# Optimization experiments

Measured on AMD Instinct MI355X. Metric: run time of the kernel, lower is better.

## Reference

```python
import jax, jax.numpy as jnp
import numpy as np
import math

D_MODEL = 1024
N_HEADS = 16
D_K = D_MODEL // N_HEADS
THETA = 0.1


def setup_inputs() -> dict:
    key = jax.random.key(0)
    ks = jax.random.split(key, 6)
    scale = np.sqrt(1.0 / D_MODEL).astype(np.float32)
    x = jax.random.normal(ks[0], (4, 2048, D_MODEL), dtype=jnp.float32)
    W_q = jax.random.normal(ks[1], (D_MODEL, D_MODEL), dtype=jnp.float32) * scale
    W_k = jax.random.normal(ks[2], (D_MODEL, D_MODEL), dtype=jnp.float32) * scale
    W_v = jax.random.normal(ks[3], (D_MODEL, D_MODEL), dtype=jnp.float32) * scale
    W_o = jax.random.normal(ks[4], (D_MODEL, D_MODEL), dtype=jnp.float32) * scale
    alpha = jnp.ones((1,), dtype=jnp.float32)
    return {"x": x, "W_q": W_q, "W_k": W_k, "W_v": W_v, "W_o": W_o, "alpha": alpha}


def reference(x, W_q, W_k, W_v, W_o, alpha):
    B, S, _ = x.shape
    Q = x @ W_q
    K = x @ W_k
    V = x @ W_v
    # non-commutative elementwise transforms
    Q = Q + THETA * jnp.sin(Q)
    K = K + THETA * jnp.cos(K)
    V = V + alpha * THETA * jnp.tanh(V)
    # split heads: [B, H, S, d_k]
    def split(t):
        return t.reshape(B, S, N_HEADS, D_K).transpose(0, 2, 1, 3)
    Qh, Kh, Vh = split(Q), split(K), split(V)
    scores = jnp.einsum('bhqd,bhkd->bhqk', Qh, Kh) / math.sqrt(D_K)
    attn = jax.nn.softmax(scores, axis=-1)
    out = jnp.einsum('bhqk,bhkd->bhqd', attn, Vh)
    out = out.transpose(0, 2, 1, 3).reshape(B, S, D_MODEL)
    return out @ W_o
```

## Files before the change

kernel.cpp:

```cpp
#include <hip/hip_runtime.h>

typedef __bf16 bf16x8 __attribute__((ext_vector_type(8)));
typedef float f32x4 __attribute__((ext_vector_type(4)));
typedef float f32x16 __attribute__((ext_vector_type(16)));

#define MFMA16(a,b,c) __builtin_amdgcn_mfma_f32_16x16x32_bf16(a,b,c,0,0,0)
#define MFMA32(a,b,c) __builtin_amdgcn_mfma_f32_32x32x16_bf16(a,b,c,0,0,0)

__device__ __forceinline__ unsigned short f2bf(float f) {
  unsigned int u = __float_as_uint(f);
  u = (u + 0x7FFFu + ((u >> 16) & 1u)) >> 16;
  return (unsigned short)u;
}

__device__ __forceinline__ void gload16(const void* g, void* l) {
  __builtin_amdgcn_global_load_lds(
      (const __attribute__((address_space(1))) void*)g,
      (__attribute__((address_space(3))) void*)l, 16, 0, 0);
}

__device__ __forceinline__ float vexp2(float x) {
  float r;
  asm("v_exp_f32 %0, %1" : "=v"(r) : "v"(x));
  return r;
}

__device__ __forceinline__ bf16x8 mk_pfrag(int hi, float p0, float p1, float p2, float p3,
                                           float p4, float p5, float p6, float p7) {
  unsigned int a0, a1, b0, b1;
  asm("v_cvt_pk_bf16_f32 %0, %1, %2" : "=v"(a0) : "v"(p0), "v"(p1));
  asm("v_cvt_pk_bf16_f32 %0, %1, %2" : "=v"(a1) : "v"(p2), "v"(p3));
  asm("v_cvt_pk_bf16_f32 %0, %1, %2" : "=v"(b0) : "v"(p4), "v"(p5));
  asm("v_cvt_pk_bf16_f32 %0, %1, %2" : "=v"(b1) : "v"(p6), "v"(p7));
  unsigned int x = __shfl_xor(hi ? a0 : b0, 32);
  unsigned int y = __shfl_xor(hi ? a1 : b1, 32);
  uint4 w;
  w.x = hi ? x : a0;
  w.y = hi ? y : a1;
  w.z = hi ? b0 : x;
  w.w = hi ? b1 : y;
  return *reinterpret_cast<bf16x8*>(&w);
}

__global__ __launch_bounds__(256) void k_convx(const float* __restrict__ x,
                                               unsigned short* __restrict__ xb) {
  int i = (blockIdx.x * 256 + threadIdx.x) * 4;
  float4 v = *reinterpret_cast<const float4*>(x + i);
  ushort4 o;
  o.x = f2bf(v.x); o.y = f2bf(v.y); o.z = f2bf(v.z); o.w = f2bf(v.w);
  *reinterpret_cast<ushort4*>(xb + i) = o;
}

__global__ __launch_bounds__(256) void k_transw(const float* __restrict__ W,
                                                unsigned short* __restrict__ WT) {
  __shared__ float t[32][33];
  int bx = blockIdx.x * 32;
  int by = blockIdx.y * 32;
  int tx = threadIdx.x & 31;
  int ty = threadIdx.x >> 5;
#pragma unroll
  for (int i = 0; i < 32; i += 8)
    t[ty + i][tx] = W[(size_t)(by + ty + i) * 1024 + bx + tx];
  __syncthreads();
#pragma unroll
  for (int i = 0; i < 32; i += 8)
    WT[(size_t)(bx + ty + i) * 1024 + by + tx] = f2bf(t[tx][ty + i]);
}

template <int EPI>
__global__ __launch_bounds__(256) void k_gemm(
    const unsigned short* __restrict__ A, const unsigned short* __restrict__ BT, int K,
    unsigned short* __restrict__ Qf, unsigned short* __restrict__ Kf,
    unsigned short* __restrict__ Vf, const float* __restrict__ alphaPtr,
    float* __restrict__ Out) {
  __shared__ __align__(16) unsigned short smem[128 * 136];
  unsigned short* AsBase = smem;
  unsigned short* BsBase = smem + 128 * 32;
  const int tid = threadIdx.x;
  const int wave = tid >> 6, lane = tid & 63;
  const int l15 = lane & 15, lg = lane >> 4;
  const int wr = wave >> 1, wc = wave & 1;
  const int bm = blockIdx.x, bn = blockIdx.y;

  f32x4 acc[4][4] = {};
  const unsigned short* Ab = A + (size_t)bm * 128 * K;
  const unsigned short* Bb = BT + (size_t)bn * 128 * K;

  const int r0 = tid >> 2, q0 = (tid & 3) * 8;
  const int r1 = r0 + 64;
  char* ldsA = (char*)AsBase + wave * 1024;
  char* ldsB = (char*)BsBase + wave * 1024;

  for (int k0 = 0; k0 < K; k0 += 32) {
    gload16((const void*)(Ab + (size_t)r0 * K + k0 + q0), ldsA);
    gload16((const void*)(Ab + (size_t)r1 * K + k0 + q0), ldsA + 4096);
    gload16((const void*)(Bb + (size_t)r0 * K + k0 + q0), ldsB);
    gload16((const void*)(Bb + (size_t)r1 * K + k0 + q0), ldsB + 4096);
    __syncthreads();
    bf16x8 af[4], bfr[4];
#pragma unroll
    for (int mi = 0; mi < 4; ++mi)
      af[mi] = *reinterpret_cast<const bf16x8*>(&AsBase[(wr * 64 + mi * 16 + l15) * 32 + lg * 8]);
#pragma unroll
    for (int ni = 0; ni < 4; ++ni)
      bfr[ni] = *reinterpret_cast<const bf16x8*>(&BsBase[(wc * 64 + ni * 16 + l15) * 32 + lg * 8]);
#pragma unroll
    for (int mi = 0; mi < 4; ++mi)
#pragma unroll
      for (int ni = 0; ni < 4; ++ni)
        acc[mi][ni] = MFMA16(af[mi], bfr[ni], acc[mi][ni]);
    __syncthreads();
  }

  if (EPI == 0) {
    const float av = alphaPtr[0];
    const int t = bn >> 3;
#pragma unroll
    for (int mi = 0; mi < 4; ++mi)
#pragma unroll
      for (int ni = 0; ni < 4; ++ni)
#pragma unroll
        for (int r = 0; r < 4; ++r) {
          int row = wr * 64 + mi * 16 + lg * 4 + r;
          int col = wc * 64 + ni * 16 + l15;
          float v = acc[mi][ni][r];
          if (t == 0) v += 0.1f * __sinf(v);
          else if (t == 1) v += 0.1f * __cosf(v);
          else {
            float e = __expf(2.0f * v);
            v += av * 0.1f * (1.0f - 2.0f * __builtin_amdgcn_rcpf(e + 1.0f));
          }
          smem[row * 136 + col] = f2bf(v);
        }
    __syncthreads();
    unsigned short* dst = (t == 0) ? Qf : (t == 1) ? Kf : Vf;
    const int c16 = tid & 15, rb = tid >> 4;
    const int ncol0 = (bn & 7) * 128;
#pragma unroll
    for (int i2 = 0; i2 < 8; ++i2) {
      int srow = rb + i2 * 16;
      uint4 val = *reinterpret_cast<const uint4*>(&smem[srow * 136 + c16 * 8]);
      *reinterpret_cast<uint4*>(dst + (size_t)(bm * 128 + srow) * 1024 + ncol0 + c16 * 8) = val;
    }
  } else {
#pragma unroll
    for (int ni = 0; ni < 4; ++ni) {
      int n = bn * 128 + wc * 64 + ni * 16 + l15;
#pragma unroll
      for (int mi = 0; mi < 4; ++mi) {
        int row = bm * 128 + wr * 64 + mi * 16 + lg * 4;
#pragma unroll
        for (int r = 0; r < 4; ++r)
          Out[(size_t)(row + r) * 1024 + n] = acc[mi][ni][r];
      }
    }
  }
}

__global__ __launch_bounds__(256)
__attribute__((amdgpu_waves_per_eu(4, 4)))
void k_attn(const unsigned short* __restrict__ Qf,
            const unsigned short* __restrict__ Kf,
            const unsigned short* __restrict__ Vf,
            unsigned short* __restrict__ AO) {
  __shared__ __align__(16) unsigned short smem[2 * (4096 + 4608)];
  const int tid = threadIdx.x;
  const int wave = tid >> 6, lane = tid & 63;
  const int l31 = lane & 31, hi = lane >> 5;
  const int f = (blockIdx.y << 4) | blockIdx.x;
  const int nf = ((f & 7) << 7) | (f >> 3);
  const int qb = nf & 15, bh = nf >> 4;
  const int b = bh >> 4, h = bh & 15;

  const unsigned short* Qb = Qf + ((size_t)b * 2048 + qb * 128 + wave * 32) * 1024 + h * 64;
  const unsigned short* Kb = Kf + (size_t)b * 2048 * 1024 + h * 64;
  const unsigned short* Vb = Vf + (size_t)b * 2048 * 1024 + h * 64;

  bf16x8 qfr[4];
#pragma unroll
  for (int ds = 0; ds < 4; ++ds)
    qfr[ds] = *reinterpret_cast<const bf16x8*>(Qb + (size_t)l31 * 1024 + ds * 16 + hi * 8);

  float lsum = 0.f;
  f32x16 o0 = {}, o1 = {};

  const int krow0 = wave * 16 + (lane >> 3);
  const int ksrcc = ((lane & 7) ^ (lane >> 3)) << 3;
  const int kxor = l31 & 7;

  const int sr = tid >> 3, sc = (tid & 7) * 8;
  const int u8 = tid & 7;
  const int swz0 = (l31 >> 3) << 3;
  const int swz1 = ((l31 >> 3) ^ 4) << 3;

  const float C1 = 0.18033688011112042f;

  uint4 va0, va1;
  va0 = *reinterpret_cast<const uint4*>(Vb + (size_t)sr * 1024 + sc);
  va1 = *reinterpret_cast<const uint4*>(Vb + (size_t)(sr + 32) * 1024 + sc);

  {
    unsigned short* Ks = smem;
    unsigned short* VT = smem + 4096;
    gload16((const void*)(Kb + (size_t)krow0 * 1024 + ksrcc), (char*)Ks + wave * 2048);
    gload16((const void*)(Kb + (size_t)(krow0 + 8) * 1024 + ksrcc), (char*)Ks + wave * 2048 + 1024);
    unsigned int w0[4] = {va0.x, va0.y, va0.z, va0.w};
    unsigned int w1[4] = {va1.x, va1.y, va1.z, va1.w};
#pragma unroll
    for (int e = 0; e < 4; ++e) {
      int d = sc + 2 * e;
      VT[(d * 72 + sr) ^ (u8 << 3)] = (unsigned short)w0[e];
      VT[((d + 1) * 72 + sr) ^ (u8 << 3)] = (unsigned short)(w0[e] >> 16);
      VT[(d * 72 + sr + 32) ^ (u8 << 3)] = (unsigned short)w1[e];
      VT[((d + 1) * 72 + sr + 32) ^ (u8 << 3)] = (unsigned short)(w1[e] >> 16);
    }
  }
  __syncthreads();

  for (int t = 0; t < 32; ++t) {
    unsigned short* KsC = smem + (t & 1) * 8704;
    unsigned short* VTC = KsC + 4096;
    unsigned short* KsN = smem + ((t + 1) & 1) * 8704;
    unsigned short* VTN = KsN + 4096;

    if (t < 31) {
      int kn = (t + 1) * 64;
      gload16((const void*)(Kb + (size_t)(kn + krow0) * 1024 + ksrcc), (char*)KsN + wave * 2048);
      gload16((const void*)(Kb + (size_t)(kn + krow0 + 8) * 1024 + ksrcc),
              (char*)KsN + wave * 2048 + 1024);
      va0 = *reinterpret_cast<const uint4*>(Vb + (size_t)(kn + sr) * 1024 + sc);
      va1 = *reinterpret_cast<const uint4*>(Vb + (size_t)(kn + sr + 32) * 1024 + sc);
    }

    f32x16 s0 = {}, s1 = {};
    __builtin_amdgcn_s_setprio(1);
#pragma unroll
    for (int ds = 0; ds < 4; ++ds) {
      int ch = ((ds * 2 + hi) ^ kxor) * 8;
      bf16x8 kf0 = *reinterpret_cast<const bf16x8*>(&KsC[l31 * 64 + ch]);
      bf16x8 kf1 = *reinterpret_cast<const bf16x8*>(&KsC[(l31 + 32) * 64 + ch]);
      s0 = MFMA32(kf0, qfr[ds], s0);
      s1 = MFMA32(kf1, qfr[ds], s1);
    }
    __builtin_amdgcn_s_setprio(0);

    float rs0 = 0.f, rs1 = 0.f, rs2 = 0.f, rs3 = 0.f;
#pragma unroll
    for (int r = 0; r < 16; r += 4) {
      float p0 = vexp2(s0[r] * C1);     s0[r] = p0;     rs0 += p0;
      float p1 = vexp2(s0[r + 1] * C1); s0[r + 1] = p1; rs1 += p1;
      float p2 = vexp2(s0[r + 2] * C1); s0[r + 2] = p2; rs2 += p2;
      float p3 = vexp2(s0[r + 3] * C1); s0[r + 3] = p3; rs3 += p3;
    }
#pragma unroll
    for (int r = 0; r < 16; r += 4) {
      float p0 = vexp2(s1[r] * C1);     s1[r] = p0;     rs0 += p0;
      float p1 = vexp2(s1[r + 1] * C1); s1[r + 1] = p1; rs1 += p1;
      float p2 = vexp2(s1[r + 2] * C1); s1[r + 2] = p2; rs2 += p2;
      float p3 = vexp2(s1[r + 3] * C1); s1[r + 3] = p3; rs3 += p3;
    }
    lsum += (rs0 + rs1) + (rs2 + rs3);

    if (t < 31) {
      unsigned int w0[4] = {va0.x, va0.y, va0.z, va0.w};
      unsigned int w1[4] = {va1.x, va1.y, va1.z, va1.w};
#pragma unroll
      for (int e = 0; e < 4; ++e) {
        int d = sc + 2 * e;
        VTN[(d * 72 + sr) ^ (u8 << 3)] = (unsigned short)w0[e];
        VTN[((d + 1) * 72 + sr) ^ (u8 << 3)] = (unsigned short)(w0[e] >> 16);
        VTN[(d * 72 + sr + 32) ^ (u8 << 3)] = (unsigned short)w1[e];
        VTN[((d + 1) * 72 + sr + 32) ^ (u8 << 3)] = (unsigned short)(w1[e] >> 16);
      }
    }

    __builtin_amdgcn_s_setprio(1);
#pragma unroll
    for (int ks = 0; ks < 4; ++ks) {
      bf16x8 pf =
          (ks == 0) ? mk_pfrag(hi, s0[0], s0[1], s0[2], s0[3], s0[4], s0[5], s0[6], s0[7])
        : (ks == 1) ? mk_pfrag(hi, s0[8], s0[9], s0[10], s0[11], s0[12], s0[13], s0[14], s0[15])
        : (ks == 2) ? mk_pfrag(hi, s1[0], s1[1], s1[2], s1[3], s1[4], s1[5], s1[6], s1[7])
                    : mk_pfrag(hi, s1[8], s1[9], s1[10], s1[11], s1[12], s1[13], s1[14], s1[15]);
      bf16x8 v0 = *reinterpret_cast<const bf16x8*>(&VTC[(l31 * 72 + ks * 16 + hi * 8) ^ swz0]);
      bf16x8 v1 = *reinterpret_cast<const bf16x8*>(&VTC[((l31 + 32) * 72 + ks * 16 + hi * 8) ^ swz1]);
      o0 = MFMA32(v0, pf, o0);
      o1 = MFMA32(v1, pf, o1);
    }
    __builtin_amdgcn_s_setprio(0);
    __syncthreads();
  }

  lsum += __shfl_xor(lsum, 32);
  const float inv = 1.0f / lsum;
  unsigned short* OL = smem + wave * 2304;
#pragma unroll
  for (int r = 0; r < 16; ++r) {
    int d0 = (r & 3) + 8 * (r >> 2) + 4 * hi;
    OL[l31 * 72 + d0] = f2bf(o0[r] * inv);
    OL[l31 * 72 + 32 + d0] = f2bf(o1[r] * inv);
  }
  __syncthreads();
#pragma unroll
  for (int p = 0; p < 4; ++p) {
    int u = tid + p * 256;
    int row = u >> 3, ch = u & 7;
    uint4 val = *reinterpret_cast<const uint4*>(&smem[(row >> 5) * 2304 + (row & 31) * 72 + ch * 8]);
    *reinterpret_cast<uint4*>(AO + ((size_t)b * 2048 + qb * 128 + row) * 1024 + h * 64 + ch * 8) = val;
  }
}

extern "C" void kernel_launch(void* const* d_in, const int* in_sizes, int n_in,
                              void* d_out, int out_size, void* d_ws, size_t ws_size,
                              hipStream_t stream) {
  const float* x = (const float*)d_in[0];
  const float* Wq = (const float*)d_in[1];
  const float* Wk = (const float*)d_in[2];
  const float* Wv = (const float*)d_in[3];
  const float* Wo = (const float*)d_in[4];
  const float* alpha = (const float*)d_in[5];
  float* out = (float*)d_out;

  char* ws = (char*)d_ws;
  unsigned short* xb  = (unsigned short*)(ws);
  unsigned short* WT3 = (unsigned short*)(ws + 16777216);
  unsigned short* WoT = (unsigned short*)(ws + 23068672);
  unsigned short* Qf  = (unsigned short*)(ws + 25165824);
  unsigned short* Kf  = (unsigned short*)(ws + 41943040);
  unsigned short* Vf  = (unsigned short*)(ws + 58720256);
  unsigned short* AO  = (unsigned short*)(ws + 75497472);

  k_convx<<<dim3(8192), dim3(256), 0, stream>>>(x, xb);
  k_transw<<<dim3(32, 32), dim3(256), 0, stream>>>(Wq, WT3);
  k_transw<<<dim3(32, 32), dim3(256), 0, stream>>>(Wk, WT3 + 1024 * 1024);
  k_transw<<<dim3(32, 32), dim3(256), 0, stream>>>(Wv, WT3 + 2 * 1024 * 1024);
  k_transw<<<dim3(32, 32), dim3(256), 0, stream>>>(Wo, WoT);

  k_gemm<0><<<dim3(64, 24), dim3(256), 0, stream>>>(xb, WT3, 1024, Qf, Kf, Vf, alpha, nullptr);
  k_attn<<<dim3(16, 64), dim3(256), 0, stream>>>(Qf, Kf, Vf, AO);
  k_gemm<1><<<dim3(64, 8), dim3(256), 0, stream>>>(AO, WoT, 1024, nullptr, nullptr, nullptr, nullptr, out);
}
```

Measured before the change: 237.6 us.

## Write V pre-transposed per head from QKV GEMM and async-load it in attention

The QKV GEMM epilogue now writes V directly in a per-head transposed [b,h,d,s] layout with 4-element packed stores. The attention kernel can then stream V tiles with global_load_lds like K, instead of register loads followed by scalar LDS scatter-transposes. It also uses a swizzled 64-wide V tile and drops the waves_per_eu attribute. The cost is that the GEMM epilogue's V stores are strided, since each 8-byte store goes to a different row, and attention occupancy may change without the attribute.

```diff
diff --git a/kernel.cpp b/kernel.cpp
--- a/kernel.cpp
+++ b/kernel.cpp
@@ -71,7 +71,7 @@
 __global__ __launch_bounds__(256) void k_gemm(
     const unsigned short* __restrict__ A, const unsigned short* __restrict__ BT, int K,
     unsigned short* __restrict__ Qf, unsigned short* __restrict__ Kf,
-    unsigned short* __restrict__ Vf, const float* __restrict__ alphaPtr,
+    unsigned short* __restrict__ VT, const float* __restrict__ alphaPtr,
     float* __restrict__ Out) {
   __shared__ __align__(16) unsigned short smem[128 * 136];
   unsigned short* AsBase = smem;
@@ -115,32 +115,50 @@
   if (EPI == 0) {
     const float av = alphaPtr[0];
     const int t = bn >> 3;
-#pragma unroll
-    for (int mi = 0; mi < 4; ++mi)
-#pragma unroll
-      for (int ni = 0; ni < 4; ++ni)
-#pragma unroll
-        for (int r = 0; r < 4; ++r) {
-          int row = wr * 64 + mi * 16 + lg * 4 + r;
-          int col = wc * 64 + ni * 16 + l15;
-          float v = acc[mi][ni][r];
-          if (t == 0) v += 0.1f * __sinf(v);
-          else if (t == 1) v += 0.1f * __cosf(v);
-          else {
+    if (t == 2) {
+#pragma unroll
+      for (int mi = 0; mi < 4; ++mi) {
+        int row0 = bm * 128 + wr * 64 + mi * 16 + lg * 4;
+        int bb = row0 >> 11, s = row0 & 2047;
+#pragma unroll
+        for (int ni = 0; ni < 4; ++ni) {
+          int col = (bn & 7) * 128 + wc * 64 + ni * 16 + l15;
+          int hh = col >> 6, dd = col & 63;
+          ushort4 pk;
+#pragma unroll
+          for (int r = 0; r < 4; ++r) {
+            float v = acc[mi][ni][r];
             float e = __expf(2.0f * v);
             v += av * 0.1f * (1.0f - 2.0f * __builtin_amdgcn_rcpf(e + 1.0f));
+            ((unsigned short*)&pk)[r] = f2bf(v);
           }
-          smem[row * 136 + col] = f2bf(v);
+          *reinterpret_cast<ushort4*>(VT + ((size_t)(bb * 16 + hh) * 64 + dd) * 2048 + s) = pk;
         }
-    __syncthreads();
-    unsigned short* dst = (t == 0) ? Qf : (t == 1) ? Kf : Vf;
-    const int c16 = tid & 15, rb = tid >> 4;
-    const int ncol0 = (bn & 7) * 128;
-#pragma unroll
-    for (int i2 = 0; i2 < 8; ++i2) {
-      int srow = rb + i2 * 16;
-      uint4 val = *reinterpret_cast<const uint4*>(&smem[srow * 136 + c16 * 8]);
-      *reinterpret_cast<uint4*>(dst + (size_t)(bm * 128 + srow) * 1024 + ncol0 + c16 * 8) = val;
+      }
+    } else {
+#pragma unroll
+      for (int mi = 0; mi < 4; ++mi)
+#pragma unroll
+        for (int ni = 0; ni < 4; ++ni)
+#pragma unroll
+          for (int r = 0; r < 4; ++r) {
+            int row = wr * 64 + mi * 16 + lg * 4 + r;
+            int col = wc * 64 + ni * 16 + l15;
+            float v = acc[mi][ni][r];
+            if (t == 0) v += 0.1f * __sinf(v);
+            else v += 0.1f * __cosf(v);
+            smem[row * 136 + col] = f2bf(v);
+          }
+      __syncthreads();
+      unsigned short* dst = (t == 0) ? Qf : Kf;
+      const int c16 = tid & 15, rb = tid >> 4;
+      const int ncol0 = (bn & 7) * 128;
+#pragma unroll
+      for (int i2 = 0; i2 < 8; ++i2) {
+        int srow = rb + i2 * 16;
+        uint4 val = *reinterpret_cast<const uint4*>(&smem[srow * 136 + c16 * 8]);
+        *reinterpret_cast<uint4*>(dst + (size_t)(bm * 128 + srow) * 1024 + ncol0 + c16 * 8) = val;
+      }
     }
   } else {
 #pragma unroll
@@ -158,12 +176,11 @@
 }
 
 __global__ __launch_bounds__(256)
-__attribute__((amdgpu_waves_per_eu(4, 4)))
 void k_attn(const unsigned short* __restrict__ Qf,
             const unsigned short* __restrict__ Kf,
-            const unsigned short* __restrict__ Vf,
+            const unsigned short* __restrict__ VT,
             unsigned short* __restrict__ AO) {
-  __shared__ __align__(16) unsigned short smem[2 * (4096 + 4608)];
+  __shared__ __align__(16) unsigned short smem[2 * 8192];
   const int tid = threadIdx.x;
   const int wave = tid >> 6, lane = tid & 63;
   const int l31 = lane & 31, hi = lane >> 5;
@@ -174,7 +191,7 @@
 
   const unsigned short* Qb = Qf + ((size_t)b * 2048 + qb * 128 + wave * 32) * 1024 + h * 64;
   const unsigned short* Kb = Kf + (size_t)b * 2048 * 1024 + h * 64;
-  const unsigned short* Vb = Vf + (size_t)b * 2048 * 1024 + h * 64;
+  const unsigned short* Vb = VT + (size_t)bh * 64 * 2048;
 
   bf16x8 qfr[4];
 #pragma unroll
@@ -188,39 +205,21 @@
   const int ksrcc = ((lane & 7) ^ (lane >> 3)) << 3;
   const int kxor = l31 & 7;
 
-  const int sr = tid >> 3, sc = (tid & 7) * 8;
-  const int u8 = tid & 7;
-  const int swz0 = (l31 >> 3) << 3;
-  const int swz1 = ((l31 >> 3) ^ 4) << 3;
-
   const float C1 = 0.18033688011112042f;
 
-  uint4 va0, va1;
-  va0 = *reinterpret_cast<const uint4*>(Vb + (size_t)sr * 1024 + sc);
-  va1 = *reinterpret_cast<const uint4*>(Vb + (size_t)(sr + 32) * 1024 + sc);
-
   {
-    unsigned short* Ks = smem;
-    unsigned short* VT = smem + 4096;
-    gload16((const void*)(Kb + (size_t)krow0 * 1024 + ksrcc), (char*)Ks + wave * 2048);
-    gload16((const void*)(Kb + (size_t)(krow0 + 8) * 1024 + ksrcc), (char*)Ks + wave * 2048 + 1024);
-    unsigned int w0[4] = {va0.x, va0.y, va0.z, va0.w};
-    unsigned int w1[4] = {va1.x, va1.y, va1.z, va1.w};
-#pragma unroll
-    for (int e = 0; e < 4; ++e) {
-      int d = sc + 2 * e;
-      VT[(d * 72 + sr) ^ (u8 << 3)] = (unsigned short)w0[e];
-      VT[((d + 1) * 72 + sr) ^ (u8 << 3)] = (unsigned short)(w0[e] >> 16);
-      VT[(d * 72 + sr + 32) ^ (u8 << 3)] = (unsigned short)w1[e];
-      VT[((d + 1) * 72 + sr + 32) ^ (u8 << 3)] = (unsigned short)(w1[e] >> 16);
-    }
+    gload16((const void*)(Kb + (size_t)krow0 * 1024 + ksrcc), (char*)smem + wave * 2048);
+    gload16((const void*)(Kb + (size_t)(krow0 + 8) * 1024 + ksrcc), (char*)smem + wave * 2048 + 1024);
+    gload16((const void*)(Vb + (size_t)krow0 * 2048 + ksrcc), (char*)(smem + 4096) + wave * 2048);
+    gload16((const void*)(Vb + (size_t)(krow0 + 8) * 2048 + ksrcc),
+            (char*)(smem + 4096) + wave * 2048 + 1024);
   }
   __syncthreads();
 
   for (int t = 0; t < 32; ++t) {
-    unsigned short* KsC = smem + (t & 1) * 8704;
+    unsigned short* KsC = smem + (t & 1) * 8192;
     unsigned short* VTC = KsC + 4096;
-    unsigned short* KsN = smem + ((t + 1) & 1) * 8704;
+    unsigned short* KsN = smem + ((t + 1) & 1) * 8192;
     unsigned short* VTN = KsN + 4096;
 
     if (t < 31) {
@@ -228,8 +227,9 @@
       gload16((const void*)(Kb + (size_t)(kn + krow0) * 1024 + ksrcc), (char*)KsN + wave * 2048);
       gload16((const void*)(Kb + (size_t)(kn + krow0 + 8) * 1024 + ksrcc),
               (char*)KsN + wave * 2048 + 1024);
-      va0 = *reinterpret_cast<const uint4*>(Vb + (size_t)(kn + sr) * 1024 + sc);
-      va1 = *reinterpret_cast<const uint4*>(Vb + (size_t)(kn + sr + 32) * 1024 + sc);
+      gload16((const void*)(Vb + (size_t)krow0 * 2048 + kn + ksrcc), (char*)VTN + wave * 2048);
+      gload16((const void*)(Vb + (size_t)(krow0 + 8) * 2048 + kn + ksrcc),
+              (char*)VTN + wave * 2048 + 1024);
     }
 
     f32x16 s0 = {}, s1 = {};
@@ -261,19 +261,6 @@
     }
     lsum += (rs0 + rs1) + (rs2 + rs3);
 
-    if (t < 31) {
-      unsigned int w0[4] = {va0.x, va0.y, va0.z, va0.w};
-      unsigned int w1[4] = {va1.x, va1.y, va1.z, va1.w};
-#pragma unroll
-      for (int e = 0; e < 4; ++e) {
-        int d = sc + 2 * e;
-        VTN[(d * 72 + sr) ^ (u8 << 3)] = (unsigned short)w0[e];
-        VTN[((d + 1) * 72 + sr) ^ (u8 << 3)] = (unsigned short)(w0[e] >> 16);
-        VTN[(d * 72 + sr + 32) ^ (u8 << 3)] = (unsigned short)w1[e];
-        VTN[((d + 1) * 72 + sr + 32) ^ (u8 << 3)] = (unsigned short)(w1[e] >> 16);
-      }
-    }
-
     __builtin_amdgcn_s_setprio(1);
 #pragma unroll
     for (int ks = 0; ks < 4; ++ks) {
@@ -282,8 +269,9 @@
         : (ks == 1) ? mk_pfrag(hi, s0[8], s0[9], s0[10], s0[11], s0[12], s0[13], s0[14], s0[15])
         : (ks == 2) ? mk_pfrag(hi, s1[0], s1[1], s1[2], s1[3], s1[4], s1[5], s1[6], s1[7])
                     : mk_pfrag(hi, s1[8], s1[9], s1[10], s1[11], s1[12], s1[13], s1[14], s1[15]);
-      bf16x8 v0 = *reinterpret_cast<const bf16x8*>(&VTC[(l31 * 72 + ks * 16 + hi * 8) ^ swz0]);
-      bf16x8 v1 = *reinterpret_cast<const bf16x8*>(&VTC[((l31 + 32) * 72 + ks * 16 + hi * 8) ^ swz1]);
+      int ch = ((ks * 2 + hi) ^ kxor) * 8;
+      bf16x8 v0 = *reinterpret_cast<const bf16x8*>(&VTC[l31 * 64 + ch]);
+      bf16x8 v1 = *reinterpret_cast<const bf16x8*>(&VTC[(l31 + 32) * 64 + ch]);
       o0 = MFMA32(v0, pf, o0);
       o1 = MFMA32(v1, pf, o1);
     }
@@ -327,7 +315,7 @@
   unsigned short* WoT = (unsigned short*)(ws + 23068672);
   unsigned short* Qf  = (unsigned short*)(ws + 25165824);
   unsigned short* Kf  = (unsigned short*)(ws + 41943040);
-  unsigned short* Vf  = (unsigned short*)(ws + 58720256);
+  unsigned short* VTb = (unsigned short*)(ws + 58720256);
   unsigned short* AO  = (unsigned short*)(ws + 75497472);
 
   k_convx<<<dim3(8192), dim3(256), 0, stream>>>(x, xb);
@@ -336,7 +324,7 @@
   k_transw<<<dim3(32, 32), dim3(256), 0, stream>>>(Wv, WT3 + 2 * 1024 * 1024);
   k_transw<<<dim3(32, 32), dim3(256), 0, stream>>>(Wo, WoT);
 
-  k_gemm<0><<<dim3(64, 24), dim3(256), 0, stream>>>(xb, WT3, 1024, Qf, Kf, Vf, alpha, nullptr);
-  k_attn<<<dim3(16, 64), dim3(256), 0, stream>>>(Qf, Kf, Vf, AO);
+  k_gemm<0><<<dim3(64, 24), dim3(256), 0, stream>>>(xb, WT3, 1024, Qf, Kf, VTb, alpha, nullptr);
+  k_attn<<<dim3(16, 64), dim3(256), 0, stream>>>(Qf, Kf, VTb, AO);
   k_gemm<1><<<dim3(64, 8), dim3(256), 0, stream>>>(AO, WoT, 1024, nullptr, nullptr, nullptr, nullptr, out);
 }
```

New measurement: 230.0 us. 1.03x faster.
